# Performance work log

Measured on AMD Instinct MI355X. Metric: run time of the kernel, lower is better.

## Reference

```python
import jax, jax.numpy as jnp
import numpy as np

N_NODES = 100000
N_EDGES = 1600000
D_IN = 64
D_HID = 64
D_OUT = 64


def setup_inputs() -> dict:
    key = jax.random.key(0)
    ks = jax.random.split(key, 12)
    x = jax.random.normal(ks[0], (N_NODES, D_IN), dtype=jnp.float32)
    edge_index = jax.random.randint(ks[1], (2, N_EDGES), 0, N_NODES, dtype=jnp.int64)
    batch = jnp.zeros((N_NODES,), dtype=jnp.int64)
    # Glorot-ish init for GCNConv weights; PyG stores weight as [in, out] applied as x @ W.
    def lin(k, din, dout):
        s = 1.0 / np.sqrt(din)
        return jax.random.uniform(k, (din, dout), minval=-s, maxval=s, dtype=jnp.float32)
    W1 = lin(ks[2], D_IN, D_HID);  b1 = jnp.zeros((D_HID,), jnp.float32)
    W2 = lin(ks[3], D_HID, D_HID); b2 = jnp.zeros((D_HID,), jnp.float32)
    W3 = lin(ks[4], D_HID, D_HID); b3 = jnp.zeros((D_HID,), jnp.float32)
    W4 = lin(ks[5], D_HID, D_OUT); b4 = jnp.zeros((D_OUT,), jnp.float32)
    return {"x": x, "edge_index": edge_index, "batch": batch,
            "W1": W1, "b1": b1, "W2": W2, "b2": b2,
            "W3": W3, "b3": b3, "W4": W4, "b4": b4}


def reference(x, edge_index, batch, W1, b1, W2, b2, W3, b3, W4, b4):
    N = x.shape[0]
    loops = jnp.arange(N, dtype=edge_index.dtype)
    src = jnp.concatenate([edge_index[0], loops])  # [E+N]
    dst = jnp.concatenate([edge_index[1], loops])  # [E+N]
    # Symmetric normalization: deg over A + I (in-degree at dst), norm_e = d_src^-1/2 * d_dst^-1/2
    deg = jax.ops.segment_sum(jnp.ones(src.shape, dtype=x.dtype), dst, num_segments=N)
    dis = jnp.where(deg > 0, jax.lax.rsqrt(deg), 0.0)
    norm = (dis[src] * dis[dst])[:, None]  # [E+N, 1]

    def conv(h, W, b):
        h = h @ W                                   # [N, dout]
        msg = h[src] * norm                         # gather + scale, [E+N, dout]
        return jax.ops.segment_sum(msg, dst, num_segments=N) + b

    h = jax.nn.elu(conv(x, W1, b1))   # dropout_p=0.0 -> identity
    h = jax.nn.elu(conv(h, W2, b2))
    h = jax.nn.elu(conv(h, W3, b3))
    return conv(h, W4, b4)
```

## Files before the change

kernel.cpp:

```cpp
#include <hip/hip_runtime.h>

#define NN 100000
#define NE 1600000
#define DD 64
#define BSH 9
#define BSZ 512
#define NBKT 196
#define CHUNK 8192
#define NCH ((NE + CHUNK - 1) / CHUNK)
#define CSR2_CAP (NE + 8 * (NBKT * BSZ))


__global__ __launch_bounds__(256) void k_bcount(const int* __restrict__ ei,
                                                int* __restrict__ bcnt) {
    __shared__ int h[NBKT];
    int t = threadIdx.x;
    for (int i = t; i < NBKT; i += 256) h[i] = 0;
    __syncthreads();
    int base = blockIdx.x * CHUNK;
    for (int i = t; i < CHUNK; i += 256) {
        int e = base + i;
        if (e < NE) atomicAdd(&h[ei[NE + e] >> BSH], 1);
    }
    __syncthreads();
    for (int i = t; i < NBKT; i += 256)
        if (h[i]) atomicAdd(&bcnt[i], h[i]);
}


__global__ void k_bscan(const int* __restrict__ bcnt,
                        int* __restrict__ bbase, int* __restrict__ bcur) {
    if (threadIdx.x == 0) {
        int acc = 0;
        for (int i = 0; i < NBKT; ++i) { bbase[i] = acc; bcur[i] = acc; acc += bcnt[i]; }
        bbase[NBKT] = acc;
    }
}


__global__ __launch_bounds__(256) void k_bscat(const int* __restrict__ ei,
                                               int* __restrict__ bcur,
                                               int* __restrict__ bkt) {
    __shared__ int h[NBKT], rbase[NBKT], rcur[NBKT];
    int t = threadIdx.x;
    for (int i = t; i < NBKT; i += 256) h[i] = 0;
    __syncthreads();
    int cb = blockIdx.x * CHUNK;
    int s[32], d[32];
#pragma unroll
    for (int i = 0; i < 32; ++i) {
        int e = cb + t + 256 * i;
        if (e < NE) {
            s[i] = ei[e];
            d[i] = ei[NE + e];
            atomicAdd(&h[d[i] >> BSH], 1);
        } else {
            d[i] = -1;
        }
    }
    __syncthreads();
    for (int i = t; i < NBKT; i += 256) {
        int c = h[i];
        rbase[i] = c ? atomicAdd(&bcur[i], c) : 0;
        rcur[i] = 0;
    }
    __syncthreads();
#pragma unroll
    for (int i = 0; i < 32; ++i) {
        if (d[i] >= 0) {
            int b = d[i] >> BSH;
            int pos = rbase[b] + atomicAdd(&rcur[b], 1);
            bkt[pos] = s[i] | ((d[i] & (BSZ - 1)) << 17);
        }
    }
}


__global__ __launch_bounds__(256) void k_ncnt(const int* __restrict__ bbase,
                                              const int* __restrict__ bkt,
                                              int* __restrict__ ncnt,
                                              int* __restrict__ bptot,
                                              double* __restrict__ dis) {
    __shared__ int cnt[BSZ];
    __shared__ int red[256];
    int b = blockIdx.x, t = threadIdx.x;
    cnt[t] = 0; cnt[t + 256] = 0;
    __syncthreads();
    int beg = bbase[b], end = bbase[b + 1];
    for (int j = beg + t; j < end; j += 256)
        atomicAdd(&cnt[bkt[j] >> 17], 1);
    __syncthreads();
    int nb = b * BSZ;
    int n0 = nb + t, n1 = nb + t + 256;
    int c0 = cnt[t], c1 = cnt[t + 256];
    int p0 = (n0 < NN) ? ((c0 + 8) & ~7) : 0;
    int p1 = (n1 < NN) ? ((c1 + 8) & ~7) : 0;
    if (n0 < NN) { ncnt[n0] = c0; dis[n0] = 1.0 / sqrt((double)(c0 + 1)); }
    if (n1 < NN) { ncnt[n1] = c1; dis[n1] = 1.0 / sqrt((double)(c1 + 1)); }
    red[t] = p0 + p1;
    __syncthreads();
    for (int o = 128; o > 0; o >>= 1) {
        if (t < o) red[t] += red[t + o];
        __syncthreads();
    }
    if (t == 0) bptot[b] = red[0];
}


__global__ void k_pscan(const int* __restrict__ bptot,
                        int* __restrict__ pbase, int* __restrict__ rp2) {
    if (threadIdx.x == 0) {
        int acc = 0;
        for (int i = 0; i < NBKT; ++i) { pbase[i] = acc; acc += bptot[i]; }
        rp2[NN] = acc;
    }
}


__global__ __launch_bounds__(256) void k_bfill(const int* __restrict__ bbase,
                                               const int* __restrict__ bkt,
                                               const int* __restrict__ ncnt,
                                               const int* __restrict__ pbase,
                                               int* __restrict__ rp2,
                                               int* __restrict__ csr2) {
    __shared__ int cur[BSZ];
    __shared__ int s2[256];
    int b = blockIdx.x, t = threadIdx.x;
    int nb = b * BSZ;
    int gbase = pbase[b];
    int n0 = nb + 2 * t, n1 = nb + 2 * t + 1;
    int c0 = (n0 < NN) ? ncnt[n0] : -1;
    int c1 = (n1 < NN) ? ncnt[n1] : -1;
    int q0 = (c0 >= 0) ? ((c0 + 8) & ~7) : 0;
    int q1 = (c1 >= 0) ? ((c1 + 8) & ~7) : 0;
    s2[t] = q0 + q1;
    __syncthreads();
    for (int o = 1; o < 256; o <<= 1) {
        int v = (t >= o) ? s2[t - o] : 0;
        __syncthreads();
        s2[t] += v;
        __syncthreads();
    }
    int ex = s2[t] - (q0 + q1);
    if (c0 >= 0) { int g = gbase + ex;      rp2[n0] = g; csr2[g] = n0; cur[2 * t]     = ex + 1; }
    if (c1 >= 0) { int g = gbase + ex + q0; rp2[n1] = g; csr2[g] = n1; cur[2 * t + 1] = ex + q0 + 1; }
    __syncthreads();
    int beg = bbase[b], end = bbase[b + 1];
    for (int j = beg + t; j < end; j += 256) {
        int pk = bkt[j];
        int pos = gbase + atomicAdd(&cur[pk >> 17], 1);
        csr2[pos] = pk & 0x1FFFF;
    }
    __syncthreads();
    if (c0 >= 0) { int e0 = ex + q0;      for (int j = cur[2 * t];     j < e0; ++j) csr2[gbase + j] = NN; }
    if (c1 >= 0) { int e1 = ex + q0 + q1; for (int j = cur[2 * t + 1]; j < e1; ++j) csr2[gbase + j] = NN; }
}


__global__ __launch_bounds__(256) void k_gemm(const float* __restrict__ in,
                                              const float* __restrict__ W,
                                              const double* __restrict__ dis,
                                              float* __restrict__ h2s) {
    __shared__ float sW[DD * DD];
    __shared__ float sIn[128 * 65];
    int t = threadIdx.x;
    int brow = blockIdx.x * 128;
#pragma unroll
    for (int i = 0; i < 16; ++i) sW[t + 256 * i] = W[t + 256 * i];
#pragma unroll
    for (int i = 0; i < 32; ++i) {
        int idx = t + 256 * i;
        int rr = idx >> 6, kk = idx & 63;
        int gr = brow + rr; if (gr >= NN) gr = NN - 1;
        sIn[rr * 65 + kk] = in[(size_t)gr * DD + kk];
    }
    __syncthreads();
    int cg = t & 7;
    int rg = t >> 3;
    const float* sInB = &sIn[rg * 4 * 65];

    float aE[4][8], aO[4][8];
#pragma unroll
    for (int i = 0; i < 4; ++i)
#pragma unroll
        for (int j = 0; j < 8; ++j) { aE[i][j] = 0.f; aO[i][j] = 0.f; }

#pragma unroll 4
    for (int k = 0; k < DD; k += 2) {
        float4 w0 = *(const float4*)&sW[k * DD + cg * 8];
        float4 w1 = *(const float4*)&sW[k * DD + cg * 8 + 4];
        float4 w2 = *(const float4*)&sW[(k + 1) * DD + cg * 8];
        float4 w3 = *(const float4*)&sW[(k + 1) * DD + cg * 8 + 4];
        float wv0[8] = {w0.x, w0.y, w0.z, w0.w, w1.x, w1.y, w1.z, w1.w};
        float wv1[8] = {w2.x, w2.y, w2.z, w2.w, w3.x, w3.y, w3.z, w3.w};
#pragma unroll
        for (int i = 0; i < 4; ++i) {
            float a0 = sInB[i * 65 + k];
            float a1 = sInB[i * 65 + k + 1];
#pragma unroll
            for (int j = 0; j < 8; ++j) {
                aE[i][j] = fmaf(a0, wv0[j], aE[i][j]);
                aO[i][j] = fmaf(a1, wv1[j], aO[i][j]);
            }
        }
    }

#pragma unroll
    for (int i = 0; i < 4; ++i) {
        int row = brow + rg * 4 + i;
        if (row < NN) {
            double dr = dis[row];
            float o[8];
#pragma unroll
            for (int j = 0; j < 8; ++j)
                o[j] = (float)((double)(aE[i][j] + aO[i][j]) * dr);
            *(float4*)&h2s[(size_t)row * DD + cg * 8]     = make_float4(o[0], o[1], o[2], o[3]);
            *(float4*)&h2s[(size_t)row * DD + cg * 8 + 4] = make_float4(o[4], o[5], o[6], o[7]);
        }
    }
}


__global__ __launch_bounds__(256) void k_aggr(const int* __restrict__ rp2,
                                              const int* __restrict__ csr2,
                                              const float* __restrict__ h2s,
                                              const double* __restrict__ dis,
                                              const float* __restrict__ b,
                                              float* __restrict__ out,
                                              int apply_elu) {
    int gid = blockIdx.x * 256 + threadIdx.x;
    int node = gid >> 6;
    int lane = gid & 63;
    int beg = __builtin_amdgcn_readfirstlane(rp2[node]);
    int end = __builtin_amdgcn_readfirstlane(rp2[node + 1]);
    double a0 = 0.0, a1 = 0.0;
    for (int j = beg; j < end; j += 8) {
        int4 i0 = *(const int4*)&csr2[j];
        int4 i1 = *(const int4*)&csr2[j + 4];
        float v0 = h2s[(size_t)(unsigned)i0.x * DD + lane];
        float v1 = h2s[(size_t)(unsigned)i0.y * DD + lane];
        float v2 = h2s[(size_t)(unsigned)i0.z * DD + lane];
        float v3 = h2s[(size_t)(unsigned)i0.w * DD + lane];
        float v4 = h2s[(size_t)(unsigned)i1.x * DD + lane];
        float v5 = h2s[(size_t)(unsigned)i1.y * DD + lane];
        float v6 = h2s[(size_t)(unsigned)i1.z * DD + lane];
        float v7 = h2s[(size_t)(unsigned)i1.w * DD + lane];
        a0 += (double)v0; a1 += (double)v1;
        a0 += (double)v2; a1 += (double)v3;
        a0 += (double)v4; a1 += (double)v5;
        a0 += (double)v6; a1 += (double)v7;
    }
    float vf = (float)(dis[node] * (a0 + a1) + (double)b[lane]);
    if (apply_elu && vf <= 0.f) vf = expm1f(vf);
    out[gid] = vf;
}


static inline size_t align256(size_t x) { return (x + 255) & ~(size_t)255; }

extern "C" void kernel_launch(void* const* d_in, const int* in_sizes, int n_in,
                              void* d_out, int out_size, void* d_ws, size_t ws_size,
                              hipStream_t stream) {
    const float* x  = (const float*)d_in[0];
    const int*   ei = (const int*)d_in[1];
    const float* W1 = (const float*)d_in[3];
    const float* b1 = (const float*)d_in[4];
    const float* W2 = (const float*)d_in[5];
    const float* b2 = (const float*)d_in[6];
    const float* W3 = (const float*)d_in[7];
    const float* b3 = (const float*)d_in[8];
    const float* W4 = (const float*)d_in[9];
    const float* b4 = (const float*)d_in[10];
    float* out = (float*)d_out;

    char* ws = (char*)d_ws;
    size_t off = 0;
    double* dis   = (double*)(ws + off); off = align256(off + (size_t)NN * sizeof(double));
    float*  h2s   = (float*) (ws + off); off = align256(off + (size_t)(NN + 1) * DD * sizeof(float));
    float*  A     = (float*) (ws + off); off = align256(off + (size_t)NN * DD * sizeof(float));
    int*    ncnt  = (int*)   (ws + off); off = align256(off + (size_t)NN * sizeof(int));
    int*    rp2   = (int*)   (ws + off); off = align256(off + (size_t)(NN + 1) * sizeof(int));
    int*    bcnt  = (int*)   (ws + off); off = align256(off + (size_t)(NBKT + 1) * sizeof(int));
    int*    bbase = (int*)   (ws + off); off = align256(off + (size_t)(NBKT + 1) * sizeof(int));
    int*    bcur  = (int*)   (ws + off); off = align256(off + (size_t)(NBKT + 1) * sizeof(int));
    int*    bptot = (int*)   (ws + off); off = align256(off + (size_t)(NBKT + 1) * sizeof(int));
    int*    pbase = (int*)   (ws + off); off = align256(off + (size_t)(NBKT + 1) * sizeof(int));
    int*    bkt   = (int*)   (ws + off); off = align256(off + (size_t)NE * sizeof(int));
    int*    csr2  = (int*)   (ws + off); off = align256(off + (size_t)CSR2_CAP * sizeof(int));

    hipMemsetAsync(bcnt, 0, (size_t)NBKT * sizeof(int), stream);
    hipMemsetAsync(h2s + (size_t)NN * DD, 0, DD * sizeof(float), stream);

    k_bcount<<<NCH, 256, 0, stream>>>(ei, bcnt);
    k_bscan<<<1, 64, 0, stream>>>(bcnt, bbase, bcur);
    k_bscat<<<NCH, 256, 0, stream>>>(ei, bcur, bkt);
    k_ncnt<<<NBKT, 256, 0, stream>>>(bbase, bkt, ncnt, bptot, dis);
    k_pscan<<<1, 64, 0, stream>>>(bptot, pbase, rp2);
    k_bfill<<<NBKT, 256, 0, stream>>>(bbase, bkt, ncnt, pbase, rp2, csr2);

    struct Layer { const float* in; const float* b; const float* W; float* o; int elu; };
    Layer L[4] = {
        { x,   b1, W1, A,   1 },
        { A,   b2, W2, out, 1 },
        { out, b3, W3, A,   1 },
        { A,   b4, W4, out, 0 },
    };

    for (int l = 0; l < 4; ++l) {
        k_gemm<<<(NN + 127) / 128, 256, 0, stream>>>(L[l].in, L[l].W, dis, h2s);
        k_aggr<<<NN / 4, 256, 0, stream>>>(rp2, csr2, h2s, dis, L[l].b, L[l].o, L[l].elu);
    }
}
```

Before: 395.2 us.

## Pad CSR rows to 16 and unroll aggregation by 16; parallelize bucket scans

Rows of the padded CSR are now rounded up to multiples of 16 instead of 8, so the aggregation kernel can issue 16 independent neighbor gathers per iteration with four double accumulators, raising memory-level parallelism. The two single-thread serial prefix scans over buckets are replaced with 256-thread shared-memory Hillis-Steele scans. The cost is more padding slots that gather the zero row, which adds wasted loads for the average degree of about 17, and a larger CSR buffer.

```diff
diff --git a/kernel.cpp b/kernel.cpp
--- a/kernel.cpp
+++ b/kernel.cpp
@@ -8,7 +8,7 @@
 #define NBKT 196
 #define CHUNK 8192
 #define NCH ((NE + CHUNK - 1) / CHUNK)
-#define CSR2_CAP (NE + 8 * (NBKT * BSZ))
+#define CSR2_CAP (NE + 16 * (NBKT * BSZ))
 
 
 __global__ __launch_bounds__(256) void k_bcount(const int* __restrict__ ei,
@@ -28,13 +28,23 @@
 }
 
 
-__global__ void k_bscan(const int* __restrict__ bcnt,
-                        int* __restrict__ bbase, int* __restrict__ bcur) {
-    if (threadIdx.x == 0) {
-        int acc = 0;
-        for (int i = 0; i < NBKT; ++i) { bbase[i] = acc; bcur[i] = acc; acc += bcnt[i]; }
-        bbase[NBKT] = acc;
-    }
+__global__ __launch_bounds__(256) void k_bscan(const int* __restrict__ bcnt,
+                                               int* __restrict__ bbase,
+                                               int* __restrict__ bcur) {
+    __shared__ int s[256];
+    int t = threadIdx.x;
+    int v = (t < NBKT) ? bcnt[t] : 0;
+    s[t] = v;
+    __syncthreads();
+    for (int o = 1; o < 256; o <<= 1) {
+        int x = (t >= o) ? s[t - o] : 0;
+        __syncthreads();
+        s[t] += x;
+        __syncthreads();
+    }
+    int ex = s[t] - v;
+    if (t < NBKT) { bbase[t] = ex; bcur[t] = ex; }
+    if (t == NBKT) bbase[NBKT] = ex;
 }
 
 
@@ -93,8 +103,8 @@
     int nb = b * BSZ;
     int n0 = nb + t, n1 = nb + t + 256;
     int c0 = cnt[t], c1 = cnt[t + 256];
-    int p0 = (n0 < NN) ? ((c0 + 8) & ~7) : 0;
-    int p1 = (n1 < NN) ? ((c1 + 8) & ~7) : 0;
+    int p0 = (n0 < NN) ? ((c0 + 16) & ~15) : 0;
+    int p1 = (n1 < NN) ? ((c1 + 16) & ~15) : 0;
     if (n0 < NN) { ncnt[n0] = c0; dis[n0] = 1.0 / sqrt((double)(c0 + 1)); }
     if (n1 < NN) { ncnt[n1] = c1; dis[n1] = 1.0 / sqrt((double)(c1 + 1)); }
     red[t] = p0 + p1;
@@ -107,13 +117,23 @@
 }
 
 
-__global__ void k_pscan(const int* __restrict__ bptot,
-                        int* __restrict__ pbase, int* __restrict__ rp2) {
-    if (threadIdx.x == 0) {
-        int acc = 0;
-        for (int i = 0; i < NBKT; ++i) { pbase[i] = acc; acc += bptot[i]; }
-        rp2[NN] = acc;
-    }
+__global__ __launch_bounds__(256) void k_pscan(const int* __restrict__ bptot,
+                                               int* __restrict__ pbase,
+                                               int* __restrict__ rp2) {
+    __shared__ int s[256];
+    int t = threadIdx.x;
+    int v = (t < NBKT) ? bptot[t] : 0;
+    s[t] = v;
+    __syncthreads();
+    for (int o = 1; o < 256; o <<= 1) {
+        int x = (t >= o) ? s[t - o] : 0;
+        __syncthreads();
+        s[t] += x;
+        __syncthreads();
+    }
+    int ex = s[t] - v;
+    if (t < NBKT) pbase[t] = ex;
+    if (t == NBKT) rp2[NN] = ex;
 }
 
 
@@ -131,8 +151,8 @@
     int n0 = nb + 2 * t, n1 = nb + 2 * t + 1;
     int c0 = (n0 < NN) ? ncnt[n0] : -1;
     int c1 = (n1 < NN) ? ncnt[n1] : -1;
-    int q0 = (c0 >= 0) ? ((c0 + 8) & ~7) : 0;
-    int q1 = (c1 >= 0) ? ((c1 + 8) & ~7) : 0;
+    int q0 = (c0 >= 0) ? ((c0 + 16) & ~15) : 0;
+    int q1 = (c1 >= 0) ? ((c1 + 16) & ~15) : 0;
     s2[t] = q0 + q1;
     __syncthreads();
     for (int o = 1; o < 256; o <<= 1) {
@@ -233,24 +253,35 @@
     int lane = gid & 63;
     int beg = __builtin_amdgcn_readfirstlane(rp2[node]);
     int end = __builtin_amdgcn_readfirstlane(rp2[node + 1]);
-    double a0 = 0.0, a1 = 0.0;
-    for (int j = beg; j < end; j += 8) {
+    double a0 = 0.0, a1 = 0.0, a2 = 0.0, a3 = 0.0;
+    for (int j = beg; j < end; j += 16) {
         int4 i0 = *(const int4*)&csr2[j];
         int4 i1 = *(const int4*)&csr2[j + 4];
-        float v0 = h2s[(size_t)(unsigned)i0.x * DD + lane];
-        float v1 = h2s[(size_t)(unsigned)i0.y * DD + lane];
-        float v2 = h2s[(size_t)(unsigned)i0.z * DD + lane];
-        float v3 = h2s[(size_t)(unsigned)i0.w * DD + lane];
-        float v4 = h2s[(size_t)(unsigned)i1.x * DD + lane];
-        float v5 = h2s[(size_t)(unsigned)i1.y * DD + lane];
-        float v6 = h2s[(size_t)(unsigned)i1.z * DD + lane];
-        float v7 = h2s[(size_t)(unsigned)i1.w * DD + lane];
-        a0 += (double)v0; a1 += (double)v1;
-        a0 += (double)v2; a1 += (double)v3;
-        a0 += (double)v4; a1 += (double)v5;
-        a0 += (double)v6; a1 += (double)v7;
-    }
-    float vf = (float)(dis[node] * (a0 + a1) + (double)b[lane]);
+        int4 i2 = *(const int4*)&csr2[j + 8];
+        int4 i3 = *(const int4*)&csr2[j + 12];
+        float v0  = h2s[(size_t)(unsigned)i0.x * DD + lane];
+        float v1  = h2s[(size_t)(unsigned)i0.y * DD + lane];
+        float v2  = h2s[(size_t)(unsigned)i0.z * DD + lane];
+        float v3  = h2s[(size_t)(unsigned)i0.w * DD + lane];
+        float v4  = h2s[(size_t)(unsigned)i1.x * DD + lane];
+        float v5  = h2s[(size_t)(unsigned)i1.y * DD + lane];
+        float v6  = h2s[(size_t)(unsigned)i1.z * DD + lane];
+        float v7  = h2s[(size_t)(unsigned)i1.w * DD + lane];
+        float v8  = h2s[(size_t)(unsigned)i2.x * DD + lane];
+        float v9  = h2s[(size_t)(unsigned)i2.y * DD + lane];
+        float v10 = h2s[(size_t)(unsigned)i2.z * DD + lane];
+        float v11 = h2s[(size_t)(unsigned)i2.w * DD + lane];
+        float v12 = h2s[(size_t)(unsigned)i3.x * DD + lane];
+        float v13 = h2s[(size_t)(unsigned)i3.y * DD + lane];
+        float v14 = h2s[(size_t)(unsigned)i3.z * DD + lane];
+        float v15 = h2s[(size_t)(unsigned)i3.w * DD + lane];
+        a0 += (double)v0;  a1 += (double)v1;  a2 += (double)v2;  a3 += (double)v3;
+        a0 += (double)v4;  a1 += (double)v5;  a2 += (double)v6;  a3 += (double)v7;
+        a0 += (double)v8;  a1 += (double)v9;  a2 += (double)v10; a3 += (double)v11;
+        a0 += (double)v12; a1 += (double)v13; a2 += (double)v14; a3 += (double)v15;
+    }
+    double sum = (a0 + a1) + (a2 + a3);
+    float vf = (float)(dis[node] * sum + (double)b[lane]);
     if (apply_elu && vf <= 0.f) vf = expm1f(vf);
     out[gid] = vf;
 }
@@ -292,10 +323,10 @@
     hipMemsetAsync(h2s + (size_t)NN * DD, 0, DD * sizeof(float), stream);
 
     k_bcount<<<NCH, 256, 0, stream>>>(ei, bcnt);
-    k_bscan<<<1, 64, 0, stream>>>(bcnt, bbase, bcur);
+    k_bscan<<<1, 256, 0, stream>>>(bcnt, bbase, bcur);
     k_bscat<<<NCH, 256, 0, stream>>>(ei, bcur, bkt);
     k_ncnt<<<NBKT, 256, 0, stream>>>(bbase, bkt, ncnt, bptot, dis);
-    k_pscan<<<1, 64, 0, stream>>>(bptot, pbase, rp2);
+    k_pscan<<<1, 256, 0, stream>>>(bptot, pbase, rp2);
     k_bfill<<<NBKT, 256, 0, stream>>>(bbase, bkt, ncnt, pbase, rp2, csr2);
 
     struct Layer { const float* in; const float* b; const float* W; float* o; int elu; };
```

Result: faster. 386.9 us (-2.1%).
